# Kernel tuning notes

Hardware: AMD Instinct MI355X
Metric: run time of the kernel (lower is better)

The kernel has to match this reference:

```python
import jax, jax.numpy as jnp
import numpy as np

B, T = 32, 128
V, E, H = 32000, 512, 1024
SOS_IDX = 1


def setup_inputs() -> dict:
    key = jax.random.key(0)
    ks = jax.random.split(key, 9)
    s = lambda n: 1.0 / np.sqrt(n)
    return {
        "target": jax.random.randint(ks[0], (B, T), 0, V, dtype=jnp.int64),
        "h0": jax.random.normal(ks[1], (B, H), dtype=jnp.float32),
        "emb": jax.random.normal(ks[2], (V, E), dtype=jnp.float32),
        "W_ih": jax.random.normal(ks[3], (H, E), dtype=jnp.float32) * s(E),
        "b_ih": jax.random.normal(ks[4], (H,), dtype=jnp.float32) * s(E),
        "W_hh": jax.random.normal(ks[5], (H, H), dtype=jnp.float32) * s(H),
        "b_hh": jax.random.normal(ks[6], (H,), dtype=jnp.float32) * s(H),
        "W_out": jax.random.normal(ks[7], (V, H), dtype=jnp.float32) * s(H),
        "b_out": jax.random.normal(ks[8], (V,), dtype=jnp.float32) * s(H),
    }


def reference(target, h0, emb, W_ih, b_ih, W_hh, b_hh, W_out, b_out):
    # Teacher-forcing ratio fixed at 1.0 (deterministic): input tokens are
    # [sos, target[:,1], ..., target[:,T-1]] per the original `target[:, t+1]`.
    Bb, Tt = target.shape
    sos = jnp.full((Bb, 1), SOS_IDX, dtype=target.dtype)
    tokens = jnp.concatenate([sos, target[:, 1:]], axis=1)  # (B, T)
    x = emb[tokens]  # (B, T, E) -- embedding gather done once, vectorized

    def step(h, x_t):
        # manual RNN cell: h' = tanh(x W_ih^T + b_ih + h W_hh^T + b_hh)
        h = jnp.tanh(x_t @ W_ih.T + b_ih + h @ W_hh.T + b_hh)  # (B, H)
        out = h @ W_out.T + b_out  # (B, V) linear decode
        return h, out

    _, outs = jax.lax.scan(step, h0, jnp.swapaxes(x, 0, 1))  # (T, B, V)
    return jnp.swapaxes(outs, 0, 1)  # (B, T, V)
```

## Files before the change

kernel.cpp:

```cpp
#include <hip/hip_runtime.h>
#include <stdint.h>

#define T_SEQ 128
#define B_SZ  32
#define H_DIM 1024
#define E_DIM 512
#define V_DIM 32000
#define SOS_TOK 1
#define NCONS 448
#define NTILES 8000

typedef float v4f __attribute__((ext_vector_type(4)));
typedef short short8 __attribute__((ext_vector_type(8)));

__device__ inline uint16_t f2bf(float x) {
    uint32_t u = __float_as_uint(x);
    uint32_t r = (u + 0x7fffu + ((u >> 16) & 1u)) >> 16;
    return (uint16_t)r;
}
__device__ inline uint32_t pack2(float a, float b) {
    return (uint32_t)f2bf(a) | ((uint32_t)f2bf(b) << 16);
}

__device__ inline void gload16(const void* g, void* l) {
    __builtin_amdgcn_global_load_lds(
        (const __attribute__((address_space(1))) uint32_t*)g,
        (__attribute__((address_space(3))) uint32_t*)l, 16, 0, 0);
}

__global__ __launch_bounds__(256) void kconv(const float* __restrict__ W,
                                             uint16_t* __restrict__ Wb) {
    size_t i = ((size_t)blockIdx.x * 256 + threadIdx.x) * 8;
    float4 a = *(const float4*)&W[i];
    float4 c = *(const float4*)&W[i + 4];
    uint4 p;
    p.x = pack2(a.x, a.y); p.y = pack2(a.z, a.w);
    p.z = pack2(c.x, c.y); p.w = pack2(c.z, c.w);
    *(uint4*)&Wb[i] = p;
}

__global__ __launch_bounds__(256) void kxwm(const int* __restrict__ target,
                                            const float* __restrict__ emb,
                                            const float* __restrict__ Wih,
                                            const float* __restrict__ bih,
                                            const float* __restrict__ bhh,
                                            float* __restrict__ xW) {
    __shared__ __align__(16) uint16_t As[128 * 32];
    __shared__ __align__(16) uint16_t Bs[128 * 32];
    __shared__ int toks[128];
    int m0 = blockIdx.x * 128, n0 = blockIdx.y * 128;
    int tid = threadIdx.x;
    if (tid < 128) {
        int row = m0 + tid;
        int t = row & (T_SEQ - 1);
        toks[tid] = (t == 0) ? SOS_TOK : target[row];
    }
    __syncthreads();

    v4f acc[4][4] = {};
    int lane = tid & 63, wv = tid >> 6, wm = wv >> 1, wn = wv & 1;
    int ar = lane & 15, ko = (lane >> 4) * 8;

    for (int k0 = 0; k0 < E_DIM; k0 += 32) {
#pragma unroll
        for (int l = 0; l < 2; ++l) {
            int c = tid + l * 256;
            int r = c >> 2, ko8 = (c & 3) * 8;
            const float* asrc = &emb[(size_t)toks[r] * E_DIM + k0 + ko8];
            float4 x = *(const float4*)asrc;
            float4 y = *(const float4*)(asrc + 4);
            uint4 p;
            p.x = pack2(x.x, x.y); p.y = pack2(x.z, x.w);
            p.z = pack2(y.x, y.y); p.w = pack2(y.z, y.w);
            *(uint4*)&As[r * 32 + ko8] = p;
            const float* bsrc = &Wih[(size_t)(n0 + r) * E_DIM + k0 + ko8];
            float4 u = *(const float4*)bsrc;
            float4 v = *(const float4*)(bsrc + 4);
            uint4 q;
            q.x = pack2(u.x, u.y); q.y = pack2(u.z, u.w);
            q.z = pack2(v.x, v.y); q.w = pack2(v.z, v.w);
            *(uint4*)&Bs[r * 32 + ko8] = q;
        }
        __syncthreads();

        short8 a[4], bfr[4];
#pragma unroll
        for (int i = 0; i < 4; ++i)
            a[i] = *(const short8*)&As[(wm * 64 + i * 16 + ar) * 32 + ko];
#pragma unroll
        for (int jj = 0; jj < 4; ++jj)
            bfr[jj] = *(const short8*)&Bs[(wn * 64 + jj * 16 + ar) * 32 + ko];
#pragma unroll
        for (int i = 0; i < 4; ++i)
#pragma unroll
            for (int jj = 0; jj < 4; ++jj)
                acc[i][jj] = __builtin_amdgcn_mfma_f32_16x16x32_bf16(
                    a[i], bfr[jj], acc[i][jj], 0, 0, 0);
        __syncthreads();
    }

    int fr = lane & 15, fq = lane >> 4;
#pragma unroll
    for (int jj = 0; jj < 4; ++jj) {
        int col = n0 + wn * 64 + jj * 16 + fr;
        float bias = bih[col] + bhh[col];
#pragma unroll
        for (int i = 0; i < 4; ++i) {
            int row = m0 + wm * 64 + i * 16 + fq * 4;
#pragma unroll
            for (int q = 0; q < 4; ++q) {
                int m = row + q;
                int b = m >> 7, t = m & (T_SEQ - 1);
                xW[((size_t)t * B_SZ + b) * H_DIM + col] = acc[i][jj][q] + bias;
            }
        }
    }
}

template <bool BBF>
__global__ __launch_bounds__(256) void kfused(const uint16_t* __restrict__ hbInit,
                                              const uint16_t* __restrict__ WbHH,
                                              const float* __restrict__ xW,
                                              uint16_t* __restrict__ Hb,
                                              uint32_t* __restrict__ flags,
                                              const void* __restrict__ Bop,
                                              const float* __restrict__ bout,
                                              float* __restrict__ out) {
    __shared__ __align__(16) uint16_t As[128 * 32];
    __shared__ __align__(16) uint16_t Bs[128 * 32];
    int tid = threadIdx.x;
    int lane = tid & 63;

    if (blockIdx.x < 32) {
        __builtin_amdgcn_s_setprio(1);
        int blk = blockIdx.x;
        int bg = blk & 1, ngg = blk >> 1;
        int w = tid >> 6;
        int ncol0 = ngg * 64 + w * 16;
        int lr = lane & 15, lk = (lane >> 4) * 8;

        short8 wf[32];
        const uint16_t* wrow = WbHH + (size_t)(ncol0 + lr) * H_DIM + lk;
#pragma unroll
        for (int kt = 0; kt < 32; ++kt)
            wf[kt] = *(const short8*)(wrow + (size_t)kt * 32);

        int brow = bg * 16 + lr;
        int eb = bg * 16 + (lane >> 4) * 4;
        int en = ncol0 + lr;
        uint32_t* Hb32 = (uint32_t*)Hb;
        uint32_t* myflag = flags + (size_t)(bg * 16 + ngg) * 32;
        const uint32_t* grpflags = flags + (size_t)(bg * 16) * 32;

        for (int t = 0; t < T_SEQ; ++t) {
            const uint16_t* arow =
                ((t == 0) ? hbInit : Hb + (size_t)(t - 1) * B_SZ * H_DIM)
                + (size_t)brow * H_DIM + lk;

            float xv[4];
#pragma unroll
            for (int q = 0; q < 4; ++q)
                xv[q] = xW[((size_t)t * B_SZ + eb + q) * H_DIM + en];

            v4f ac0 = {0.f,0.f,0.f,0.f}, ac1 = {0.f,0.f,0.f,0.f};
            v4f ac2 = {0.f,0.f,0.f,0.f}, ac3 = {0.f,0.f,0.f,0.f};
            short8 af0[16], af1[16];
#pragma unroll
            for (int kt = 0; kt < 16; ++kt)
                af0[kt] = *(const short8*)(arow + (size_t)kt * 32);
#pragma unroll
            for (int kt = 0; kt < 16; ++kt)
                af1[kt] = *(const short8*)(arow + 512 + (size_t)kt * 32);
#pragma unroll
            for (int kt = 0; kt < 16; ++kt) {
                v4f* a = (kt & 3) == 0 ? &ac0 : (kt & 3) == 1 ? &ac1
                        : (kt & 3) == 2 ? &ac2 : &ac3;
                *a = __builtin_amdgcn_mfma_f32_16x16x32_bf16(af0[kt], wf[kt], *a, 0, 0, 0);
            }
#pragma unroll
            for (int kt = 0; kt < 16; ++kt) {
                v4f* a = (kt & 3) == 0 ? &ac0 : (kt & 3) == 1 ? &ac1
                        : (kt & 3) == 2 ? &ac2 : &ac3;
                *a = __builtin_amdgcn_mfma_f32_16x16x32_bf16(af1[kt], wf[16 + kt], *a, 0, 0, 0);
            }
            v4f acc = (ac0 + ac1) + (ac2 + ac3);

            float hv[4];
#pragma unroll
            for (int q = 0; q < 4; ++q)
                hv[q] = tanhf(acc[q] + xv[q]);

#pragma unroll
            for (int q = 0; q < 4; ++q) {
                float pv = __shfl_xor(hv[q], 1);
                bool mine = ((lane & 1) == 0) ? (q < 2) : (q >= 2);
                if (mine) {
                    uint32_t word = (lane & 1) ? pack2(pv, hv[q]) : pack2(hv[q], pv);
                    size_t i32 = (((size_t)t * B_SZ + eb + q) * H_DIM
                                  + (size_t)(en & ~1)) >> 1;
                    __hip_atomic_store(&Hb32[i32], word, __ATOMIC_RELAXED,
                                       __HIP_MEMORY_SCOPE_AGENT);
                }
            }

            __syncthreads();
            if (tid == 0)
                __hip_atomic_store(myflag, (uint32_t)(t + 1), __ATOMIC_RELEASE,
                                   __HIP_MEMORY_SCOPE_AGENT);
            if (t < T_SEQ - 1) {
                if (tid < 16) {
                    const uint32_t* f = grpflags + (size_t)tid * 32;
                    while (__hip_atomic_load(f, __ATOMIC_RELAXED,
                                             __HIP_MEMORY_SCOPE_AGENT) <= (uint32_t)t)
                        __builtin_amdgcn_s_sleep(2);
                }
                if (tid == 0)
                    (void)__hip_atomic_load(myflag, __ATOMIC_ACQUIRE,
                                            __HIP_MEMORY_SCOPE_AGENT);
                __syncthreads();
            }
        }
    } else {
        int c = blockIdx.x - 32;
        int wv = tid >> 6, wm = wv >> 1, wn = wv & 1;
        int ar = lane & 15, ko = (lane >> 4) * 8;
        int sx = BBF ? (((ar >> 1) & 3) << 3) : 0;
        int fr = lane & 15, fq = lane >> 4;
        int gate_seen = 0;
        const uint32_t* proxyf = flags + (size_t)(c & 31) * 32;

        const uint16_t* Bb = (const uint16_t*)Bop;
        const float*    Bf = (const float*)Bop;

        for (int g = c; g < NTILES; g += NCONS) {
            int mtp = g / 250, nt = g - mtp * 250;
            int need = 4 * mtp + 4;
            if (need > gate_seen) {
                if (tid == 0) {
                    while (__hip_atomic_load(proxyf, __ATOMIC_RELAXED,
                                             __HIP_MEMORY_SCOPE_AGENT) < (uint32_t)need)
                        __builtin_amdgcn_s_sleep(32);
                }
                __syncthreads();
                if (tid < 32) {
                    const uint32_t* f = flags + (size_t)tid * 32;
                    while (__hip_atomic_load(f, __ATOMIC_RELAXED,
                                             __HIP_MEMORY_SCOPE_AGENT) < (uint32_t)need)
                        __builtin_amdgcn_s_sleep(2);
                }
                __syncthreads();
                if (tid == 0)
                    (void)__hip_atomic_load(flags, __ATOMIC_ACQUIRE,
                                            __HIP_MEMORY_SCOPE_AGENT);
                __syncthreads();
                gate_seen = need;
            }

            int m0 = mtp * 128, n0 = nt * 128;
            v4f acc[4][4] = {};

            for (int k0 = 0; k0 < H_DIM; k0 += 32) {
                int wb = tid & ~63;
                if constexpr (BBF) {
#pragma unroll
                    for (int l = 0; l < 2; ++l) {
                        int cc = tid + l * 256;
                        int r = cc >> 2;
                        int gsw = ((cc & 3) ^ ((cc >> 3) & 3)) * 8;
                        gload16(&Hb[(size_t)(m0 + r) * H_DIM + k0 + gsw],
                                (char*)As + (size_t)(wb + l * 256) * 16);
                        gload16(&Bb[(size_t)(n0 + r) * H_DIM + k0 + gsw],
                                (char*)Bs + (size_t)(wb + l * 256) * 16);
                    }
                } else {
#pragma unroll
                    for (int l = 0; l < 2; ++l) {
                        int cc = tid + l * 256;
                        int r = cc >> 2, ko8 = (cc & 3) * 8;
                        gload16(&Hb[(size_t)(m0 + r) * H_DIM + k0 + ko8],
                                (char*)As + (size_t)(wb + l * 256) * 16);
                        const float* src = &Bf[(size_t)(n0 + r) * H_DIM + k0 + ko8];
                        float4 x = *(const float4*)src;
                        float4 y = *(const float4*)(src + 4);
                        uint4 p;
                        p.x = pack2(x.x, x.y); p.y = pack2(x.z, x.w);
                        p.z = pack2(y.x, y.y); p.w = pack2(y.z, y.w);
                        *(uint4*)&Bs[r * 32 + ko8] = p;
                    }
                }
                __syncthreads();

                short8 a[4], bfr[4];
#pragma unroll
                for (int i = 0; i < 4; ++i)
                    a[i] = *(const short8*)&As[(wm * 64 + i * 16 + ar) * 32 + (ko ^ sx)];
#pragma unroll
                for (int jj = 0; jj < 4; ++jj)
                    bfr[jj] = *(const short8*)&Bs[(wn * 64 + jj * 16 + ar) * 32 + (ko ^ sx)];
#pragma unroll
                for (int i = 0; i < 4; ++i)
#pragma unroll
                    for (int jj = 0; jj < 4; ++jj)
                        acc[i][jj] = __builtin_amdgcn_mfma_f32_16x16x32_bf16(
                            a[i], bfr[jj], acc[i][jj], 0, 0, 0);
                __syncthreads();
            }

#pragma unroll
            for (int jj = 0; jj < 4; ++jj) {
                int col = n0 + wn * 64 + jj * 16 + fr;
                float bo = bout[col];
#pragma unroll
                for (int i = 0; i < 4; ++i) {
                    int rbase = wm * 64 + i * 16 + fq * 4;
#pragma unroll
                    for (int q = 0; q < 4; ++q) {
                        int mp = m0 + rbase + q;
                        int tt = mp >> 5, bb = mp & 31;
                        out[((size_t)bb * T_SEQ + tt) * V_DIM + col] =
                            acc[i][jj][q] + bo;
                    }
                }
            }
        }
    }
}

extern "C" void kernel_launch(void* const* d_in, const int* in_sizes, int n_in,
                              void* d_out, int out_size, void* d_ws, size_t ws_size,
                              hipStream_t stream) {
    const int*   target = (const int*)d_in[0];
    const float* h0     = (const float*)d_in[1];
    const float* emb    = (const float*)d_in[2];
    const float* Wih    = (const float*)d_in[3];
    const float* bih    = (const float*)d_in[4];
    const float* Whh    = (const float*)d_in[5];
    const float* bhh    = (const float*)d_in[6];
    const float* Wout   = (const float*)d_in[7];
    const float* bout   = (const float*)d_in[8];
    float* out = (float*)d_out;

    char* ws = (char*)d_ws;
    float*    xW     = (float*)(ws);
    uint16_t* WbHH   = (uint16_t*)(ws + 16777216);
    uint16_t* hbInit = (uint16_t*)(ws + 18874368);
    uint32_t* flags  = (uint32_t*)(ws + 18939904);
    uint16_t* Hb     = (uint16_t*)(ws + 18944000);
    uint16_t* WbOut  = (uint16_t*)(ws + 27332608);
    const bool wbok = ws_size >= 92868608ull;

    kconv<<<512, 256, 0, stream>>>(Whh, WbHH);
    kconv<<<16, 256, 0, stream>>>(h0, hbInit);
    kxwm<<<dim3(32, 8), 256, 0, stream>>>(target, emb, Wih, bih, bhh, xW);
    hipMemsetAsync(flags, 0, 4096, stream);

    if (wbok) {
        kconv<<<16000, 256, 0, stream>>>(Wout, WbOut);
        kfused<true><<<32 + NCONS, 256, 0, stream>>>(hbInit, WbHH, xW, Hb, flags,
                                                     (const void*)WbOut, bout, out);
    } else {
        kfused<false><<<32 + NCONS, 256, 0, stream>>>(hbInit, WbHH, xW, Hb, flags,
                                                      (const void*)Wout, bout, out);
    }
}
```

Baseline: 1.167 ms.

## Halve recurrent producer blocks, each computing two column tiles per wave

Measured after the change: 1.646 ms. 41.0% more time.

```diff
diff --git a/kernel.cpp b/kernel.cpp
--- a/kernel.cpp
+++ b/kernel.cpp
@@ -7,6 +7,7 @@
 #define E_DIM 512
 #define V_DIM 32000
 #define SOS_TOK 1
+#define NPROD 16
 #define NCONS 448
 #define NTILES 8000
 
@@ -131,39 +132,47 @@
     int tid = threadIdx.x;
     int lane = tid & 63;
 
-    if (blockIdx.x < 32) {
+    if (blockIdx.x < NPROD) {
         __builtin_amdgcn_s_setprio(1);
         int blk = blockIdx.x;
         int bg = blk & 1, ngg = blk >> 1;
         int w = tid >> 6;
-        int ncol0 = ngg * 64 + w * 16;
+        int ncol0 = ngg * 128 + w * 32;
         int lr = lane & 15, lk = (lane >> 4) * 8;
 
-        short8 wf[32];
-        const uint16_t* wrow = WbHH + (size_t)(ncol0 + lr) * H_DIM + lk;
-#pragma unroll
-        for (int kt = 0; kt < 32; ++kt)
-            wf[kt] = *(const short8*)(wrow + (size_t)kt * 32);
+        short8 wf0[32], wf1[32];
+        const uint16_t* wr0 = WbHH + (size_t)(ncol0 + lr) * H_DIM + lk;
+        const uint16_t* wr1 = WbHH + (size_t)(ncol0 + 16 + lr) * H_DIM + lk;
+#pragma unroll
+        for (int kt = 0; kt < 32; ++kt) {
+            wf0[kt] = *(const short8*)(wr0 + (size_t)kt * 32);
+            wf1[kt] = *(const short8*)(wr1 + (size_t)kt * 32);
+        }
 
         int brow = bg * 16 + lr;
         int eb = bg * 16 + (lane >> 4) * 4;
-        int en = ncol0 + lr;
+        int en0 = ncol0 + lr, en1 = en0 + 16;
         uint32_t* Hb32 = (uint32_t*)Hb;
-        uint32_t* myflag = flags + (size_t)(bg * 16 + ngg) * 32;
-        const uint32_t* grpflags = flags + (size_t)(bg * 16) * 32;
+        uint32_t* myflag = flags + (size_t)(bg * 8 + ngg) * 32;
+        const uint32_t* grpflags = flags + (size_t)(bg * 8) * 32;
 
         for (int t = 0; t < T_SEQ; ++t) {
             const uint16_t* arow =
                 ((t == 0) ? hbInit : Hb + (size_t)(t - 1) * B_SZ * H_DIM)
                 + (size_t)brow * H_DIM + lk;
 
-            float xv[4];
-#pragma unroll
-            for (int q = 0; q < 4; ++q)
-                xv[q] = xW[((size_t)t * B_SZ + eb + q) * H_DIM + en];
-
-            v4f ac0 = {0.f,0.f,0.f,0.f}, ac1 = {0.f,0.f,0.f,0.f};
-            v4f ac2 = {0.f,0.f,0.f,0.f}, ac3 = {0.f,0.f,0.f,0.f};
+            float xv0[4], xv1[4];
+#pragma unroll
+            for (int q = 0; q < 4; ++q) {
+                size_t rbase = ((size_t)t * B_SZ + eb + q) * H_DIM;
+                xv0[q] = xW[rbase + en0];
+                xv1[q] = xW[rbase + en1];
+            }
+
+            v4f a0_0 = {0.f,0.f,0.f,0.f}, a0_1 = {0.f,0.f,0.f,0.f};
+            v4f a0_2 = {0.f,0.f,0.f,0.f}, a0_3 = {0.f,0.f,0.f,0.f};
+            v4f a1_0 = {0.f,0.f,0.f,0.f}, a1_1 = {0.f,0.f,0.f,0.f};
+            v4f a1_2 = {0.f,0.f,0.f,0.f}, a1_3 = {0.f,0.f,0.f,0.f};
             short8 af0[16], af1[16];
 #pragma unroll
             for (int kt = 0; kt < 16; ++kt)
@@ -173,33 +182,45 @@
                 af1[kt] = *(const short8*)(arow + 512 + (size_t)kt * 32);
 #pragma unroll
             for (int kt = 0; kt < 16; ++kt) {
-                v4f* a = (kt & 3) == 0 ? &ac0 : (kt & 3) == 1 ? &ac1
-                        : (kt & 3) == 2 ? &ac2 : &ac3;
-                *a = __builtin_amdgcn_mfma_f32_16x16x32_bf16(af0[kt], wf[kt], *a, 0, 0, 0);
+                v4f* p0 = (kt & 3) == 0 ? &a0_0 : (kt & 3) == 1 ? &a0_1
+                        : (kt & 3) == 2 ? &a0_2 : &a0_3;
+                v4f* p1 = (kt & 3) == 0 ? &a1_0 : (kt & 3) == 1 ? &a1_1
+                        : (kt & 3) == 2 ? &a1_2 : &a1_3;
+                *p0 = __builtin_amdgcn_mfma_f32_16x16x32_bf16(af0[kt], wf0[kt], *p0, 0, 0, 0);
+                *p1 = __builtin_amdgcn_mfma_f32_16x16x32_bf16(af0[kt], wf1[kt], *p1, 0, 0, 0);
             }
 #pragma unroll
             for (int kt = 0; kt < 16; ++kt) {
-                v4f* a = (kt & 3) == 0 ? &ac0 : (kt & 3) == 1 ? &ac1
-                        : (kt & 3) == 2 ? &ac2 : &ac3;
-                *a = __builtin_amdgcn_mfma_f32_16x16x32_bf16(af1[kt], wf[16 + kt], *a, 0, 0, 0);
-            }
-            v4f acc = (ac0 + ac1) + (ac2 + ac3);
-
-            float hv[4];
-#pragma unroll
-            for (int q = 0; q < 4; ++q)
-                hv[q] = tanhf(acc[q] + xv[q]);
-
+                v4f* p0 = (kt & 3) == 0 ? &a0_0 : (kt & 3) == 1 ? &a0_1
+                        : (kt & 3) == 2 ? &a0_2 : &a0_3;
+                v4f* p1 = (kt & 3) == 0 ? &a1_0 : (kt & 3) == 1 ? &a1_1
+                        : (kt & 3) == 2 ? &a1_2 : &a1_3;
+                *p0 = __builtin_amdgcn_mfma_f32_16x16x32_bf16(af1[kt], wf0[16 + kt], *p0, 0, 0, 0);
+                *p1 = __builtin_amdgcn_mfma_f32_16x16x32_bf16(af1[kt], wf1[16 + kt], *p1, 0, 0, 0);
+            }
+            v4f acc0 = (a0_0 + a0_1) + (a0_2 + a0_3);
+            v4f acc1 = (a1_0 + a1_1) + (a1_2 + a1_3);
+
+            float hv0[4], hv1[4];
 #pragma unroll
             for (int q = 0; q < 4; ++q) {
-                float pv = __shfl_xor(hv[q], 1);
+                hv0[q] = tanhf(acc0[q] + xv0[q]);
+                hv1[q] = tanhf(acc1[q] + xv1[q]);
+            }
+
+#pragma unroll
+            for (int q = 0; q < 4; ++q) {
+                float pv0 = __shfl_xor(hv0[q], 1);
+                float pv1 = __shfl_xor(hv1[q], 1);
                 bool mine = ((lane & 1) == 0) ? (q < 2) : (q >= 2);
                 if (mine) {
-                    uint32_t word = (lane & 1) ? pack2(pv, hv[q]) : pack2(hv[q], pv);
-                    size_t i32 = (((size_t)t * B_SZ + eb + q) * H_DIM
-                                  + (size_t)(en & ~1)) >> 1;
-                    __hip_atomic_store(&Hb32[i32], word, __ATOMIC_RELAXED,
-                                       __HIP_MEMORY_SCOPE_AGENT);
+                    size_t rbase = ((size_t)t * B_SZ + eb + q) * H_DIM;
+                    uint32_t w0 = (lane & 1) ? pack2(pv0, hv0[q]) : pack2(hv0[q], pv0);
+                    uint32_t w1 = (lane & 1) ? pack2(pv1, hv1[q]) : pack2(hv1[q], pv1);
+                    __hip_atomic_store(&Hb32[(rbase + (size_t)(en0 & ~1)) >> 1], w0,
+                                       __ATOMIC_RELAXED, __HIP_MEMORY_SCOPE_AGENT);
+                    __hip_atomic_store(&Hb32[(rbase + (size_t)(en1 & ~1)) >> 1], w1,
+                                       __ATOMIC_RELAXED, __HIP_MEMORY_SCOPE_AGENT);
                 }
             }
 
@@ -208,7 +229,7 @@
                 __hip_atomic_store(myflag, (uint32_t)(t + 1), __ATOMIC_RELEASE,
                                    __HIP_MEMORY_SCOPE_AGENT);
             if (t < T_SEQ - 1) {
-                if (tid < 16) {
+                if (tid < 8) {
                     const uint32_t* f = grpflags + (size_t)tid * 32;
                     while (__hip_atomic_load(f, __ATOMIC_RELAXED,
                                              __HIP_MEMORY_SCOPE_AGENT) <= (uint32_t)t)
@@ -221,13 +242,13 @@
             }
         }
     } else {
-        int c = blockIdx.x - 32;
+        int c = blockIdx.x - NPROD;
         int wv = tid >> 6, wm = wv >> 1, wn = wv & 1;
         int ar = lane & 15, ko = (lane >> 4) * 8;
         int sx = BBF ? (((ar >> 1) & 3) << 3) : 0;
         int fr = lane & 15, fq = lane >> 4;
         int gate_seen = 0;
-        const uint32_t* proxyf = flags + (size_t)(c & 31) * 32;
+        const uint32_t* proxyf = flags + (size_t)(c & 15) * 32;
 
         const uint16_t* Bb = (const uint16_t*)Bop;
         const float*    Bf = (const float*)Bop;
@@ -242,7 +263,7 @@
                         __builtin_amdgcn_s_sleep(32);
                 }
                 __syncthreads();
-                if (tid < 32) {
+                if (tid < 16) {
                     const uint32_t* f = flags + (size_t)tid * 32;
                     while (__hip_atomic_load(f, __ATOMIC_RELAXED,
                                              __HIP_MEMORY_SCOPE_AGENT) < (uint32_t)need)
@@ -356,10 +377,10 @@
 
     if (wbok) {
         kconv<<<16000, 256, 0, stream>>>(Wout, WbOut);
-        kfused<true><<<32 + NCONS, 256, 0, stream>>>(hbInit, WbHH, xW, Hb, flags,
-                                                     (const void*)WbOut, bout, out);
+        kfused<true><<<NPROD + NCONS, 256, 0, stream>>>(hbInit, WbHH, xW, Hb, flags,
+                                                        (const void*)WbOut, bout, out);
     } else {
-        kfused<false><<<32 + NCONS, 256, 0, stream>>>(hbInit, WbHH, xW, Hb, flags,
-                                                      (const void*)Wout, bout, out);
-    }
-}
+        kfused<false><<<NPROD + NCONS, 256, 0, stream>>>(hbInit, WbHH, xW, Hb, flags,
+                                                         (const void*)Wout, bout, out);
+    }
+}
```
